# Kernel optimization log

Hardware: AMD Instinct MI355X
Metric: run time of the kernel (lower is better)

Reference implementation:

```python
import jax, jax.numpy as jnp
import numpy as np

N_NODES = 100000
N_EDGES = 1600000
DIM = 32

def setup_inputs() -> dict:
    key = jax.random.key(0)
    k1, k2, k3, k4 = jax.random.split(key, 4)
    A_rows = jax.random.randint(k1, (N_EDGES,), 0, N_NODES, dtype=jnp.int32)
    A_cols = jax.random.randint(k2, (N_EDGES,), 0, N_NODES, dtype=jnp.int32)
    A_vals = jax.random.uniform(k3, (N_EDGES,), dtype=jnp.float32)
    x = jax.random.normal(k4, (N_NODES, DIM), dtype=jnp.float32)
    return {"A_rows": A_rows, "A_cols": A_cols, "A_vals": A_vals, "x": x}

def reference(A_rows, A_cols, A_vals, x):
    # SpMM: out[i] = sum_{e: rows[e]==i} vals[e] * x[cols[e]]
    # gather neighbor features along edges, scale by edge weight, scatter-add to rows
    msgs = A_vals[:, None] * x[A_cols]              # [E, d]
    out = jax.ops.segment_sum(msgs, A_rows, num_segments=x.shape[0])  # [n, d]
    return out
```

## Files before the change

### kernel.cpp

```cpp
#include <hip/hip_runtime.h>


#define N_NODES 100000
#define N_EDGES 1600000
#define DIM 32

#define CBR    256
#define NBC    ((N_NODES + CBR - 1) / CBR)
#define CHUNK  8
#define CAPC   6656
#define OCAP   16384

#define SC_BLOCKS   500
#define SC_THREADS  512
#define EPB         3200
#define EPT         7

#define OFF_GCNT    64
#define OFF_OVER    (OFF_GCNT + NBC * 64)
#define OFF_REGION  (((OFF_OVER + OCAP * 16) + 255) & ~255)
#define WS_NEEDED   ((size_t)OFF_REGION + (size_t)NBC * CAPC * 8)

__global__ __launch_bounds__(256) void spmm_atomic_kernel(
    const int* __restrict__ rows,
    const int* __restrict__ cols,
    const float* __restrict__ vals,
    const float* __restrict__ x,
    float* __restrict__ out)
{
    const long long idx = (long long)blockIdx.x * blockDim.x + threadIdx.x;
    const long long total = (long long)N_EDGES * DIM;
    if (idx >= total) return;

    const int e = (int)(idx >> 5);
    const int d = (int)(idx & 31);

    const int r   = rows[e];
    const int c   = cols[e];
    const float v = vals[e];

    const float xv = x[(long long)c * DIM + d];
    atomicAdd(&out[(long long)r * DIM + d], v * xv);
}

__global__ __launch_bounds__(SC_THREADS) void spmm_scatter_ws(
    const int* __restrict__ rows,
    const int* __restrict__ cols,
    const float* __restrict__ vals,
    int* __restrict__ gcnt,
    int2* __restrict__ region,
    int* __restrict__ ocount,
    int4* __restrict__ overflow)
{
    __shared__ int2 stage[EPB];
    __shared__ int  hist[NBC];
    __shared__ int  lstart[NBC];
    __shared__ int  cursor[NBC];
    __shared__ int  gbase[NBC];
    __shared__ int  scanb[SC_THREADS];

    const int tid   = threadIdx.x;
    const int ebase = blockIdx.x * EPB;

    for (int i = tid; i < NBC; i += SC_THREADS) hist[i] = 0;
    __syncthreads();

    int en_x[EPT], en_y[EPT], eb[EPT];
    #pragma unroll
    for (int i = 0; i < EPT; ++i) {
        const int o = i * SC_THREADS + tid;
        if (o < EPB) {
            const int e = ebase + o;
            const int r = rows[e];
            eb[i]   = r >> 8;
            en_x[i] = ((r & 255) << 17) | cols[e];
            en_y[i] = __float_as_int(vals[e]);
            atomicAdd(&hist[eb[i]], 1);
        } else {
            eb[i] = -1; en_x[i] = 0; en_y[i] = 0;
        }
    }
    __syncthreads();

    const int myh = (tid < NBC) ? hist[tid] : 0;
    scanb[tid] = myh;
    __syncthreads();
    for (int off = 1; off < SC_THREADS; off <<= 1) {
        int t = scanb[tid];
        if (tid >= off) t += scanb[tid - off];
        __syncthreads();
        scanb[tid] = t;
        __syncthreads();
    }
    if (tid < NBC) {
        const int excl = scanb[tid] - myh;
        lstart[tid] = excl;
        cursor[tid] = excl;
        const int pad = (myh + 7) & ~7;
        gbase[tid] = pad ? atomicAdd(&gcnt[tid * 16], pad) : 0;
    }
    __syncthreads();

    #pragma unroll
    for (int i = 0; i < EPT; ++i) {
        if (eb[i] >= 0) {
            const int p = atomicAdd(&cursor[eb[i]], 1);
            stage[p] = make_int2(en_x[i], en_y[i]);
        }
    }
    __syncthreads();

    for (int bc = tid; bc < NBC; bc += SC_THREADS) {
        const int n   = hist[bc];
        const int ls  = lstart[bc];
        const int gb  = gbase[bc];
        const int nch = (n + 7) >> 3;
        for (int jch = 0; jch < nch; ++jch) {
            const int gpos = gb + jch * CHUNK;
            if (gpos + CHUNK <= CAPC) {
                int2* dst = region + (size_t)bc * CAPC + gpos;
                #pragma unroll
                for (int j = 0; j < CHUNK; ++j) {
                    const int k = jch * CHUNK + j;
                    dst[j] = (k < n) ? stage[ls + k] : make_int2(-1, 0);
                }
            } else {
                for (int j = 0; j < CHUNK; ++j) {
                    const int k = jch * CHUNK + j;
                    if (k < n) {
                        const int2 t = stage[ls + k];
                        const int op = atomicAdd(ocount, 1);
                        if (op < OCAP)
                            overflow[op] = make_int4((bc << 8) | (t.x >> 17),
                                                     t.x & 0x1FFFF, t.y, 0);
                    }
                }
            }
        }
    }
}

__global__ __launch_bounds__(1024) void spmm_sort_gather(
    const int* __restrict__ gcnt,
    const int2* __restrict__ region,
    const float* __restrict__ x,
    float* __restrict__ out)
{
    __shared__ int2 srt[CAPC];
    __shared__ int  hist[CBR];
    __shared__ int  startx[CBR];
    __shared__ int  cursor[CBR];

    const int bc  = blockIdx.x;
    const int tid = threadIdx.x;

    int n = gcnt[bc * 16]; if (n > CAPC) n = CAPC;
    const int2* __restrict__ slice = region + (size_t)bc * CAPC;

    if (tid < CBR) hist[tid] = 0;
    __syncthreads();

    for (int k = tid; k < n; k += 1024) {
        const int xv = slice[k].x;
        if (xv >= 0) atomicAdd(&hist[xv >> 17], 1);
    }
    __syncthreads();

    int h = 0;
    if (tid < CBR) { h = hist[tid]; startx[tid] = h; }
    __syncthreads();
    for (int off = 1; off < CBR; off <<= 1) {
        int v = 0;
        if (tid < CBR) { v = startx[tid]; if (tid >= off) v += startx[tid - off]; }
        __syncthreads();
        if (tid < CBR) startx[tid] = v;
        __syncthreads();
    }
    if (tid < CBR) cursor[tid] = startx[tid] - h;
    __syncthreads();

    for (int k = tid; k < n; k += 1024) {
        const int2 e = slice[k];
        if (e.x >= 0) {
            const int p = atomicAdd(&cursor[e.x >> 17], 1);
            srt[p] = make_int2(e.x & 0x1FFFF, e.y);
        }
    }
    __syncthreads();

    const int wid  = tid >> 6;
    const int lane = tid & 63;
    const int eg   = lane >> 3;
    const int d4   = lane & 7;

    #pragma unroll
    for (int i = 0; i < 16; ++i) {
        const int lrow = wid * 16 + i;
        const int cnt  = hist[lrow];
        const int st   = startx[lrow] - cnt;

        float4 acc = make_float4(0.f, 0.f, 0.f, 0.f);
        for (int k0 = 0; k0 < cnt; k0 += 16) {
            const int ka = k0 + eg;
            const int kb = ka + 8;
            const int2 ea = (ka < cnt) ? srt[st + ka] : make_int2(0, 0);
            const int2 eb = (kb < cnt) ? srt[st + kb] : make_int2(0, 0);
            const float va = __int_as_float(ea.y);
            const float vb = __int_as_float(eb.y);
            const float4 xa = *(const float4*)&x[ea.x * DIM + d4 * 4];
            const float4 xb = *(const float4*)&x[eb.x * DIM + d4 * 4];
            acc.x = fmaf(va, xa.x, acc.x);  acc.y = fmaf(va, xa.y, acc.y);
            acc.z = fmaf(va, xa.z, acc.z);  acc.w = fmaf(va, xa.w, acc.w);
            acc.x = fmaf(vb, xb.x, acc.x);  acc.y = fmaf(vb, xb.y, acc.y);
            acc.z = fmaf(vb, xb.z, acc.z);  acc.w = fmaf(vb, xb.w, acc.w);
        }

        #pragma unroll
        for (int m = 8; m < 64; m <<= 1) {
            acc.x += __shfl_xor(acc.x, m, 64);
            acc.y += __shfl_xor(acc.y, m, 64);
            acc.z += __shfl_xor(acc.z, m, 64);
            acc.w += __shfl_xor(acc.w, m, 64);
        }

        const int r = bc * CBR + lrow;
        if (eg == 0 && r < N_NODES)
            *(float4*)&out[r * DIM + d4 * 4] = acc;
    }
}

__global__ __launch_bounds__(256) void spmm_overflow_apply(
    const int* __restrict__ ocount,
    const int4* __restrict__ overflow,
    const float* __restrict__ x,
    float* __restrict__ out)
{
    int n = *ocount;
    if (n > OCAP) n = OCAP;
    const long long total = (long long)n * DIM;
    for (long long idx = (long long)blockIdx.x * blockDim.x + threadIdx.x;
         idx < total; idx += (long long)gridDim.x * blockDim.x) {
        const int e = (int)(idx >> 5);
        const int d = (int)(idx & 31);
        const int4 t = overflow[e];
        atomicAdd(&out[(long long)t.x * DIM + d],
                  __int_as_float(t.z) * x[(long long)t.y * DIM + d]);
    }
}

extern "C" void kernel_launch(void* const* d_in, const int* in_sizes, int n_in,
                              void* d_out, int out_size, void* d_ws, size_t ws_size,
                              hipStream_t stream) {
    const int*   A_rows = (const int*)d_in[0];
    const int*   A_cols = (const int*)d_in[1];
    const float* A_vals = (const float*)d_in[2];
    const float* x      = (const float*)d_in[3];
    float*       out    = (float*)d_out;

    if (d_ws == nullptr || ws_size < WS_NEEDED) {
        hipMemsetAsync(out, 0, (size_t)out_size * sizeof(float), stream);
        const long long total = (long long)N_EDGES * DIM;
        const int block = 256;
        const long long grid = (total + block - 1) / block;
        spmm_atomic_kernel<<<(dim3)(unsigned)grid, block, 0, stream>>>(
            A_rows, A_cols, A_vals, x, out);
        return;
    }

    char* ws = (char*)d_ws;
    int*  ocount   = (int*)ws;
    int*  gcnt     = (int*)(ws + OFF_GCNT);
    int4* overflow = (int4*)(ws + OFF_OVER);
    int2* region   = (int2*)(ws + OFF_REGION);

    hipMemsetAsync(ws, 0, OFF_OVER, stream);

    spmm_scatter_ws<<<SC_BLOCKS, SC_THREADS, 0, stream>>>(
        A_rows, A_cols, A_vals, gcnt, region, ocount, overflow);

    spmm_sort_gather<<<NBC, 1024, 0, stream>>>(gcnt, region, x, out);

    spmm_overflow_apply<<<64, 256, 0, stream>>>(ocount, overflow, x, out);
}
```

Before: 136.9 us.

## Fuse overflow apply into sort-gather and use wave-shuffle scans with register-cached edges

Replaces the block-wide shared-memory Hillis-Steele scans in the scatter and sort-gather kernels with two-level wavefront shuffle scans, which need far fewer barriers. In sort-gather, each thread keeps its edges in registers after the histogram pass, so the slice is read from global memory once instead of twice. The separate overflow-apply kernel is removed and each sort-gather block applies the overflow entries for its own row bucket, saving a launch. The trade-off is that every block reads the overflow count, and if overflow occurs each block scans the whole overflow list.

After: 133.2 us. -2.7%, faster.

```diff
diff --git a/kernel.cpp b/kernel.cpp
--- a/kernel.cpp
+++ b/kernel.cpp
@@ -15,6 +15,9 @@
 #define SC_THREADS  512
 #define EPB         3200
 #define EPT         7
+
+#define SG_THREADS  1024
+#define SG_EPT      7
 
 #define OFF_GCNT    64
 #define OFF_OVER    (OFF_GCNT + NBC * 64)
@@ -57,12 +60,12 @@
     __shared__ int  lstart[NBC];
     __shared__ int  cursor[NBC];
     __shared__ int  gbase[NBC];
-    __shared__ int  scanb[SC_THREADS];
+    __shared__ int  wsum[8];
 
     const int tid   = threadIdx.x;
     const int ebase = blockIdx.x * EPB;
 
-    for (int i = tid; i < NBC; i += SC_THREADS) hist[i] = 0;
+    if (tid < NBC) hist[tid] = 0;
     __syncthreads();
 
     int en_x[EPT], en_y[EPT], eb[EPT];
@@ -82,18 +85,30 @@
     }
     __syncthreads();
 
-    const int myh = (tid < NBC) ? hist[tid] : 0;
-    scanb[tid] = myh;
-    __syncthreads();
-    for (int off = 1; off < SC_THREADS; off <<= 1) {
-        int t = scanb[tid];
-        if (tid >= off) t += scanb[tid - off];
-        __syncthreads();
-        scanb[tid] = t;
-        __syncthreads();
-    }
+    const int lane = tid & 63;
+    const int wv   = tid >> 6;
+    const int myh  = (tid < NBC) ? hist[tid] : 0;
+    int s = myh;
+    #pragma unroll
+    for (int off = 1; off < 64; off <<= 1) {
+        const int t = __shfl_up(s, off, 64);
+        if (lane >= off) s += t;
+    }
+    if (lane == 63) wsum[wv] = s;
+    __syncthreads();
+    if (wv == 0) {
+        const int t = (lane < 8) ? wsum[lane] : 0;
+        int ss = t;
+        #pragma unroll
+        for (int off = 1; off < 8; off <<= 1) {
+            const int u = __shfl_up(ss, off, 64);
+            if (lane >= off) ss += u;
+        }
+        if (lane < 8) wsum[lane] = ss - t;
+    }
+    __syncthreads();
     if (tid < NBC) {
-        const int excl = scanb[tid] - myh;
+        const int excl = s + wsum[wv] - myh;
         lstart[tid] = excl;
         cursor[tid] = excl;
         const int pad = (myh + 7) & ~7;
@@ -140,9 +155,11 @@
     }
 }
 
-__global__ __launch_bounds__(1024) void spmm_sort_gather(
+__global__ __launch_bounds__(SG_THREADS) void spmm_sort_gather(
     const int* __restrict__ gcnt,
     const int2* __restrict__ region,
+    const int* __restrict__ ocount,
+    const int4* __restrict__ overflow,
     const float* __restrict__ x,
     float* __restrict__ out)
 {
@@ -150,6 +167,7 @@
     __shared__ int  hist[CBR];
     __shared__ int  startx[CBR];
     __shared__ int  cursor[CBR];
+    __shared__ int  wsum[4];
 
     const int bc  = blockIdx.x;
     const int tid = threadIdx.x;
@@ -160,38 +178,64 @@
     if (tid < CBR) hist[tid] = 0;
     __syncthreads();
 
-    for (int k = tid; k < n; k += 1024) {
-        const int xv = slice[k].x;
-        if (xv >= 0) atomicAdd(&hist[xv >> 17], 1);
-    }
-    __syncthreads();
-
-    int h = 0;
-    if (tid < CBR) { h = hist[tid]; startx[tid] = h; }
-    __syncthreads();
-    for (int off = 1; off < CBR; off <<= 1) {
-        int v = 0;
-        if (tid < CBR) { v = startx[tid]; if (tid >= off) v += startx[tid - off]; }
-        __syncthreads();
-        if (tid < CBR) startx[tid] = v;
-        __syncthreads();
-    }
-    if (tid < CBR) cursor[tid] = startx[tid] - h;
-    __syncthreads();
-
-    for (int k = tid; k < n; k += 1024) {
-        const int2 e = slice[k];
-        if (e.x >= 0) {
-            const int p = atomicAdd(&cursor[e.x >> 17], 1);
-            srt[p] = make_int2(e.x & 0x1FFFF, e.y);
-        }
-    }
-    __syncthreads();
-
-    const int wid  = tid >> 6;
+    int ex[SG_EPT], ey[SG_EPT];
+    #pragma unroll
+    for (int i = 0; i < SG_EPT; ++i) {
+        const int k = i * SG_THREADS + tid;
+        ex[i] = -1; ey[i] = 0;
+        if (k < n) {
+            const int2 e = slice[k];
+            ex[i] = e.x; ey[i] = e.y;
+            if (e.x >= 0) atomicAdd(&hist[e.x >> 17], 1);
+        }
+    }
+    __syncthreads();
+
     const int lane = tid & 63;
-    const int eg   = lane >> 3;
-    const int d4   = lane & 7;
+    const int wv   = tid >> 6;
+    int h = 0, incl = 0;
+    if (tid < CBR) {
+        h = hist[tid];
+        int s = h;
+        #pragma unroll
+        for (int off = 1; off < 64; off <<= 1) {
+            const int t = __shfl_up(s, off, 64);
+            if (lane >= off) s += t;
+        }
+        incl = s;
+        if (lane == 63) wsum[wv] = s;
+    }
+    __syncthreads();
+    if (wv == 0) {
+        const int t = (lane < 4) ? wsum[lane] : 0;
+        int ss = t;
+        #pragma unroll
+        for (int off = 1; off < 4; off <<= 1) {
+            const int u = __shfl_up(ss, off, 64);
+            if (lane >= off) ss += u;
+        }
+        if (lane < 4) wsum[lane] = ss - t;
+    }
+    __syncthreads();
+    if (tid < CBR) {
+        incl += wsum[wv];
+        startx[tid] = incl;
+        cursor[tid] = incl - h;
+    }
+    __syncthreads();
+
+    #pragma unroll
+    for (int i = 0; i < SG_EPT; ++i) {
+        if (ex[i] >= 0) {
+            const int p = atomicAdd(&cursor[ex[i] >> 17], 1);
+            srt[p] = make_int2(ex[i] & 0x1FFFF, ey[i]);
+        }
+    }
+    __syncthreads();
+
+    const int wid = tid >> 6;
+    const int eg  = lane >> 3;
+    const int d4  = lane & 7;
 
     #pragma unroll
     for (int i = 0; i < 16; ++i) {
@@ -227,24 +271,21 @@
         if (eg == 0 && r < N_NODES)
             *(float4*)&out[r * DIM + d4 * 4] = acc;
     }
-}
-
-__global__ __launch_bounds__(256) void spmm_overflow_apply(
-    const int* __restrict__ ocount,
-    const int4* __restrict__ overflow,
-    const float* __restrict__ x,
-    float* __restrict__ out)
-{
-    int n = *ocount;
-    if (n > OCAP) n = OCAP;
-    const long long total = (long long)n * DIM;
-    for (long long idx = (long long)blockIdx.x * blockDim.x + threadIdx.x;
-         idx < total; idx += (long long)gridDim.x * blockDim.x) {
-        const int e = (int)(idx >> 5);
-        const int d = (int)(idx & 31);
-        const int4 t = overflow[e];
-        atomicAdd(&out[(long long)t.x * DIM + d],
-                  __int_as_float(t.z) * x[(long long)t.y * DIM + d]);
+
+    __syncthreads();
+    int on = *ocount;
+    if (on > 0) {
+        if (on > OCAP) on = OCAP;
+        for (int k = tid; k < on; k += SG_THREADS) {
+            const int4 t = overflow[k];
+            if ((t.x >> 8) == bc) {
+                const float v = __int_as_float(t.z);
+                const float* __restrict__ xr = x + (long long)t.y * DIM;
+                float* orow = out + (long long)t.x * DIM;
+                for (int d = 0; d < DIM; ++d)
+                    atomicAdd(&orow[d], v * xr[d]);
+            }
+        }
     }
 }
 
@@ -278,7 +319,6 @@
     spmm_scatter_ws<<<SC_BLOCKS, SC_THREADS, 0, stream>>>(
         A_rows, A_cols, A_vals, gcnt, region, ocount, overflow);
 
-    spmm_sort_gather<<<NBC, 1024, 0, stream>>>(gcnt, region, x, out);
-
-    spmm_overflow_apply<<<64, 256, 0, stream>>>(ocount, overflow, x, out);
+    spmm_sort_gather<<<NBC, SG_THREADS, 0, stream>>>(
+        gcnt, region, ocount, overflow, x, out);
 }
```
